# Performance work log

Hardware: AMD Instinct MI355X
Metric: run time of the kernel (lower is better)

## Reference

```python
import jax, jax.numpy as jnp
import numpy as np

E, T, H, I = 32, 512, 2048, 768


def setup_inputs() -> dict:
    key = jax.random.key(0)
    k1, k2, k3, k4 = jax.random.split(key, 4)
    scale = 1.0 / np.sqrt(H)
    return {
        "routed_input": jax.random.normal(k1, (E, T, H), dtype=jnp.float32),
        "gate_proj": jax.random.normal(k2, (E, I, H), dtype=jnp.float32) * scale,
        "up_proj": jax.random.normal(k3, (E, I, H), dtype=jnp.float32) * scale,
        "down_proj": jax.random.normal(k4, (E, H, I), dtype=jnp.float32) * scale,
    }


def reference(routed_input, gate_proj, up_proj, down_proj):
    # routed_input: [E, T, H]; per-expert SwiGLU MLP, concat over experts.
    gate = jnp.einsum("eth,eih->eti", routed_input, gate_proj)
    up = jnp.einsum("eth,eih->eti", routed_input, up_proj)
    hidden = jax.nn.silu(gate) * up  # [E, T, I]
    out = jnp.einsum("eti,ehi->eth", hidden, down_proj)  # [E, T, H]
    return out.reshape(E * T, H)
```

## Files before the change

kernel.cpp:

```cpp
#include <hip/hip_runtime.h>


#define NE 32
#define NT 512
#define NH 2048
#define NI 768

typedef short        short8  __attribute__((ext_vector_type(8)));
typedef float        floatx4 __attribute__((ext_vector_type(4)));
typedef __attribute__((address_space(1))) const unsigned int g_u32;
typedef __attribute__((address_space(3))) unsigned int l_u32;

__device__ __forceinline__ void gl_lds16(const void* g, void* l) {
    __builtin_amdgcn_global_load_lds((g_u32*)g, (l_u32*)l, 16, 0, 0);
}

__device__ __forceinline__ unsigned int cvt_pk_bf16(float lo, float hi) {
    unsigned int r;
    asm("v_cvt_pk_bf16_f32 %0, %1, %2" : "=v"(r) : "v"(lo), "v"(hi));
    return r;
}

__device__ __forceinline__ short8 frag8(floatx4 x0, floatx4 x1) {
    union { unsigned int u[4]; short8 s; } t;
    t.u[0] = cvt_pk_bf16(x0[0], x0[1]);
    t.u[1] = cvt_pk_bf16(x0[2], x0[3]);
    t.u[2] = cvt_pk_bf16(x1[0], x1[1]);
    t.u[3] = cvt_pk_bf16(x1[2], x1[3]);
    return t.s;
}

__device__ __forceinline__ ushort f2bf(float f) {
    union { float f; unsigned int u; } v; v.f = f;
    unsigned int r = v.u + 0x7fffu + ((v.u >> 16) & 1u);
    return (ushort)(r >> 16);
}

__global__ __launch_bounds__(512, 1) void moe_gateup(
    const float* __restrict__ rin, const float* __restrict__ gate,
    const float* __restrict__ up, ushort* __restrict__ hidden)
{
    __shared__ float S[3][3][128][32];

    const int bid = blockIdx.x;
    const int wg  = (bid & 7) * 96 + (bid >> 3);
    const int e   = wg / 24;
    const int rem = wg % 24;
    const int ti  = rem % 6;
    const int tm  = rem / 6;

    const int tid  = threadIdx.x;
    const int lane = tid & 63;
    const int wave = tid >> 6;
    const int wr = wave >> 1;
    const int wc = wave & 1;

    const float* Ab = rin  + (size_t)e * NT * NH + (size_t)(tm * 128) * NH;
    const float* Gb = gate + (size_t)e * NI * NH + (size_t)(ti * 128) * NH;
    const float* Ub = up   + (size_t)e * NI * NH + (size_t)(ti * 128) * NH;

    floatx4 accg[2][4], accu[2][4];
    #pragma unroll
    for (int m = 0; m < 2; ++m)
        #pragma unroll
        for (int n = 0; n < 4; ++n) {
            accg[m][n] = (floatx4)0.f;
            accu[m][n] = (floatx4)0.f;
        }

    const int frow = lane & 15;
    const int h    = lane >> 4;
    const int KT = NH / 32;

#define STAGE(kt, b) do {                                                    \
        const int k0_ = (kt) * 32;                                           \
        _Pragma("unroll")                                                    \
        for (int i = 0; i < 6; ++i) {                                        \
            const int idx = wave * 6 + i;                                    \
            const int t_  = idx >> 4;                                        \
            const int ri  = idx & 15;                                        \
            const int r_  = ri * 8 + (lane >> 3);                            \
            const int cs_ = (lane & 7) ^ (r_ & 7);                           \
            const float* src = (t_ == 0 ? Ab : (t_ == 1 ? Gb : Ub))          \
                               + (size_t)r_ * NH + k0_ + cs_ * 4;            \
            gl_lds16(src, &S[b][t_][ri * 8][0]);                             \
        }                                                                    \
    } while (0)

    STAGE(0, 0);
    STAGE(1, 1);

    for (int kt = 0; kt < KT; ++kt) {
        const int cur = kt % 3;
        __builtin_amdgcn_s_barrier();
        if (kt + 2 < KT) {
            STAGE(kt + 2, (kt + 2) % 3);
            asm volatile("s_waitcnt vmcnt(12)" ::: "memory");
        } else if (kt + 1 < KT) {
            asm volatile("s_waitcnt vmcnt(6)" ::: "memory");
        } else {
            asm volatile("s_waitcnt vmcnt(0)" ::: "memory");
        }
        __builtin_amdgcn_s_barrier();

        short8 af[2], gf[4], uf[4];
        #pragma unroll
        for (int m = 0; m < 2; ++m) {
            const int R = wr * 32 + m * 16 + frow;
            const int p0 = (2 * h)     ^ (R & 7);
            const int p1 = (2 * h + 1) ^ (R & 7);
            af[m] = frag8(*(const floatx4*)&S[cur][0][R][p0 * 4],
                          *(const floatx4*)&S[cur][0][R][p1 * 4]);
        }
        #pragma unroll
        for (int n = 0; n < 4; ++n) {
            const int R = wc * 64 + n * 16 + frow;
            const int p0 = (2 * h)     ^ (R & 7);
            const int p1 = (2 * h + 1) ^ (R & 7);
            gf[n] = frag8(*(const floatx4*)&S[cur][1][R][p0 * 4],
                          *(const floatx4*)&S[cur][1][R][p1 * 4]);
            uf[n] = frag8(*(const floatx4*)&S[cur][2][R][p0 * 4],
                          *(const floatx4*)&S[cur][2][R][p1 * 4]);
        }
        #pragma unroll
        for (int m = 0; m < 2; ++m)
            #pragma unroll
            for (int n = 0; n < 4; ++n) {
                accg[m][n] = __builtin_amdgcn_mfma_f32_16x16x32_bf16(
                    af[m], gf[n], accg[m][n], 0, 0, 0);
                accu[m][n] = __builtin_amdgcn_mfma_f32_16x16x32_bf16(
                    af[m], uf[n], accu[m][n], 0, 0, 0);
            }

        asm volatile("s_waitcnt lgkmcnt(0)" ::: "memory");
        __builtin_amdgcn_sched_barrier(0);
    }
#undef STAGE

    const int ccol  = lane & 15;
    const int crow0 = (lane >> 4) * 4;
    const size_t hbase = ((size_t)e * NT + (size_t)tm * 128) * NI + ti * 128;
    #pragma unroll
    for (int m = 0; m < 2; ++m)
        #pragma unroll
        for (int n = 0; n < 4; ++n)
            #pragma unroll
            for (int j = 0; j < 4; ++j) {
                const float g = accg[m][n][j];
                const float u = accu[m][n][j];
                const float hh = (g / (1.f + __expf(-g))) * u;
                const int row = wr * 32 + m * 16 + crow0 + j;
                const int col = wc * 64 + n * 16 + ccol;
                hidden[hbase + (size_t)row * NI + col] = f2bf(hh);
            }
}

__global__ __launch_bounds__(256, 2) void moe_down(
    const ushort* __restrict__ hidden, const float* __restrict__ down,
    float* __restrict__ out)
{
    __shared__ ushort As[2][128][32];
    __shared__ float  Bs[2][128][32];

    const int bid = blockIdx.x;
    const int wg  = (bid & 7) * (2048 / 8) + (bid >> 3);
    const int e   = wg >> 6;
    const int rem = wg & 63;
    const int tn  = rem & 15;
    const int tm  = rem >> 4;

    const int tid  = threadIdx.x;
    const int lane = tid & 63;
    const int wave = tid >> 6;
    const int wr = wave >> 1, wc = wave & 1;

    const ushort* Ab = hidden + ((size_t)e * NT + (size_t)tm * 128) * NI;
    const float*  Bb = down + (size_t)e * NH * NI + (size_t)(tn * 128) * NI;

    floatx4 acc[4][4];
    #pragma unroll
    for (int m = 0; m < 4; ++m)
        #pragma unroll
        for (int n = 0; n < 4; ++n) acc[m][n] = (floatx4)0.f;

    const int frow = lane & 15;
    const int h    = lane >> 4;
    const int ca   = h ^ (frow & 3);
    const int rb   = frow & 7;
    const int c0   = (2 * h) ^ rb;
    const int c1   = (2 * h + 1) ^ rb;
    const int KT = NI / 32;

#define STAGE_DN(kt, b) do {                                                 \
        const int k0_ = (kt) * 32;                                           \
        _Pragma("unroll")                                                    \
        for (int i = 0; i < 2; ++i) {                                        \
            const int g_ = wave * 2 + i;                                     \
            const int r_ = g_ * 16 + (lane >> 2);                            \
            const int cs_ = (lane & 3) ^ (r_ & 3);                           \
            gl_lds16(Ab + (size_t)r_ * NI + k0_ + cs_ * 8, &As[b][g_ * 16][0]); \
        }                                                                    \
        _Pragma("unroll")                                                    \
        for (int i = 0; i < 4; ++i) {                                        \
            const int g_ = wave * 4 + i;                                     \
            const int r_ = g_ * 8 + (lane >> 3);                             \
            const int cs_ = (lane & 7) ^ (r_ & 7);                           \
            gl_lds16(Bb + (size_t)r_ * NI + k0_ + cs_ * 4, &Bs[b][g_ * 8][0]); \
        }                                                                    \
    } while (0)

    STAGE_DN(0, 0);

    for (int kt = 0; kt < KT; ++kt) {
        const int cur = kt & 1;
        if (kt + 1 < KT) {
            STAGE_DN(kt + 1, cur ^ 1);
            asm volatile("s_waitcnt vmcnt(6)" ::: "memory");
        } else {
            asm volatile("s_waitcnt vmcnt(0)" ::: "memory");
        }
        __builtin_amdgcn_s_barrier();

        short8 af[4], bf[4];
        #pragma unroll
        for (int m = 0; m < 4; ++m) {
            const int R = wr * 64 + m * 16 + frow;
            af[m] = *(const short8*)&As[cur][R][ca * 8];
        }
        #pragma unroll
        for (int n = 0; n < 4; ++n) {
            const int R = wc * 64 + n * 16 + frow;
            bf[n] = frag8(*(const floatx4*)&Bs[cur][R][c0 * 4],
                          *(const floatx4*)&Bs[cur][R][c1 * 4]);
        }
        #pragma unroll
        for (int m = 0; m < 4; ++m)
            #pragma unroll
            for (int n = 0; n < 4; ++n)
                acc[m][n] = __builtin_amdgcn_mfma_f32_16x16x32_bf16(
                    af[m], bf[n], acc[m][n], 0, 0, 0);

        asm volatile("s_waitcnt lgkmcnt(0)" ::: "memory");
        __builtin_amdgcn_sched_barrier(0);
        __builtin_amdgcn_s_barrier();
    }
#undef STAGE_DN

    const int ccol  = lane & 15;
    const int crow0 = (lane >> 4) * 4;
    float* Ob = out + ((size_t)e * NT + (size_t)tm * 128) * NH + tn * 128;
    #pragma unroll
    for (int m = 0; m < 4; ++m)
        #pragma unroll
        for (int n = 0; n < 4; ++n)
            #pragma unroll
            for (int j = 0; j < 4; ++j) {
                const int row = wr * 64 + m * 16 + crow0 + j;
                const int col = wc * 64 + n * 16 + ccol;
                Ob[(size_t)row * NH + col] = acc[m][n][j];
            }
}

extern "C" void kernel_launch(void* const* d_in, const int* in_sizes, int n_in,
                              void* d_out, int out_size, void* d_ws, size_t ws_size,
                              hipStream_t stream) {
    const float* rin  = (const float*)d_in[0];
    const float* gate = (const float*)d_in[1];
    const float* up   = (const float*)d_in[2];
    const float* down = (const float*)d_in[3];
    float* out = (float*)d_out;
    ushort* hidden = (ushort*)d_ws;

    moe_gateup<<<dim3(768), dim3(512), 0, stream>>>(rin, gate, up, hidden);
    moe_down<<<dim3(2048), dim3(256), 0, stream>>>(hidden, down, out);
}
```

Before: 356.4 us.

## Stage gate/up GEMM operands through registers with bf16 LDS and double buffering

Replaces direct global-to-LDS fp32 async loads (triple-buffered) in the gate/up kernel with register prefetch of fp32 values, conversion to bf16 once before writing to a double-buffered LDS. This halves LDS footprint and removes the per-wave redundant fp32-to-bf16 conversions on fragment reads, allowing single short8 LDS reads per fragment. Wave tiling changes from 4x2 to 2x4 layout (64x32 per wave). Risks: register pressure from held prefetch data and reduced latency hiding versus async LDS loads.

```diff
diff --git a/kernel.cpp b/kernel.cpp
--- a/kernel.cpp
+++ b/kernel.cpp
@@ -8,6 +8,7 @@
 
 typedef short        short8  __attribute__((ext_vector_type(8)));
 typedef float        floatx4 __attribute__((ext_vector_type(4)));
+typedef unsigned int uintx4  __attribute__((ext_vector_type(4)));
 typedef __attribute__((address_space(1))) const unsigned int g_u32;
 typedef __attribute__((address_space(3))) unsigned int l_u32;
 
@@ -30,6 +31,15 @@
     return t.s;
 }
 
+__device__ __forceinline__ uintx4 pack8(floatx4 x0, floatx4 x1) {
+    uintx4 u;
+    u[0] = cvt_pk_bf16(x0[0], x0[1]);
+    u[1] = cvt_pk_bf16(x0[2], x0[3]);
+    u[2] = cvt_pk_bf16(x1[0], x1[1]);
+    u[3] = cvt_pk_bf16(x1[2], x1[3]);
+    return u;
+}
+
 __device__ __forceinline__ ushort f2bf(float f) {
     union { float f; unsigned int u; } v; v.f = f;
     unsigned int r = v.u + 0x7fffu + ((v.u >> 16) & 1u);
@@ -40,7 +50,7 @@
     const float* __restrict__ rin, const float* __restrict__ gate,
     const float* __restrict__ up, ushort* __restrict__ hidden)
 {
-    __shared__ float S[3][3][128][32];
+    __shared__ ushort S[2][3][128][32];
 
     const int bid = blockIdx.x;
     const int wg  = (bid & 7) * 96 + (bid >> 3);
@@ -52,18 +62,25 @@
     const int tid  = threadIdx.x;
     const int lane = tid & 63;
     const int wave = tid >> 6;
-    const int wr = wave >> 1;
-    const int wc = wave & 1;
+    const int wr = wave >> 2;
+    const int wc = wave & 3;
 
     const float* Ab = rin  + (size_t)e * NT * NH + (size_t)(tm * 128) * NH;
     const float* Gb = gate + (size_t)e * NI * NH + (size_t)(ti * 128) * NH;
     const float* Ub = up   + (size_t)e * NI * NH + (size_t)(ti * 128) * NH;
 
-    floatx4 accg[2][4], accu[2][4];
-    #pragma unroll
-    for (int m = 0; m < 2; ++m)
-        #pragma unroll
-        for (int n = 0; n < 4; ++n) {
+    const int s_row = wave * 16 + (lane >> 2);
+    const int s_cl  = lane & 3;
+    const int s_c   = s_cl ^ (s_row & 3);
+    const float* As_src = Ab + (size_t)s_row * NH + s_c * 8;
+    const float* Gs_src = Gb + (size_t)s_row * NH + s_c * 8;
+    const float* Us_src = Ub + (size_t)s_row * NH + s_c * 8;
+
+    floatx4 accg[4][2], accu[4][2];
+    #pragma unroll
+    for (int m = 0; m < 4; ++m)
+        #pragma unroll
+        for (int n = 0; n < 2; ++n) {
             accg[m][n] = (floatx4)0.f;
             accu[m][n] = (floatx4)0.f;
         }
@@ -72,85 +89,90 @@
     const int h    = lane >> 4;
     const int KT = NH / 32;
 
-#define STAGE(kt, b) do {                                                    \
-        const int k0_ = (kt) * 32;                                           \
-        _Pragma("unroll")                                                    \
-        for (int i = 0; i < 6; ++i) {                                        \
-            const int idx = wave * 6 + i;                                    \
-            const int t_  = idx >> 4;                                        \
-            const int ri  = idx & 15;                                        \
-            const int r_  = ri * 8 + (lane >> 3);                            \
-            const int cs_ = (lane & 7) ^ (r_ & 7);                           \
-            const float* src = (t_ == 0 ? Ab : (t_ == 1 ? Gb : Ub))          \
-                               + (size_t)r_ * NH + k0_ + cs_ * 4;            \
-            gl_lds16(src, &S[b][t_][ri * 8][0]);                             \
-        }                                                                    \
-    } while (0)
-
-    STAGE(0, 0);
-    STAGE(1, 1);
-
-    for (int kt = 0; kt < KT; ++kt) {
-        const int cur = kt % 3;
-        __builtin_amdgcn_s_barrier();
-        if (kt + 2 < KT) {
-            STAGE(kt + 2, (kt + 2) % 3);
-            asm volatile("s_waitcnt vmcnt(12)" ::: "memory");
-        } else if (kt + 1 < KT) {
-            asm volatile("s_waitcnt vmcnt(6)" ::: "memory");
-        } else {
-            asm volatile("s_waitcnt vmcnt(0)" ::: "memory");
-        }
-        __builtin_amdgcn_s_barrier();
-
-        short8 af[2], gf[4], uf[4];
-        #pragma unroll
-        for (int m = 0; m < 2; ++m) {
-            const int R = wr * 32 + m * 16 + frow;
-            const int p0 = (2 * h)     ^ (R & 7);
-            const int p1 = (2 * h + 1) ^ (R & 7);
-            af[m] = frag8(*(const floatx4*)&S[cur][0][R][p0 * 4],
-                          *(const floatx4*)&S[cur][0][R][p1 * 4]);
-        }
-        #pragma unroll
-        for (int n = 0; n < 4; ++n) {
-            const int R = wc * 64 + n * 16 + frow;
-            const int p0 = (2 * h)     ^ (R & 7);
-            const int p1 = (2 * h + 1) ^ (R & 7);
-            gf[n] = frag8(*(const floatx4*)&S[cur][1][R][p0 * 4],
-                          *(const floatx4*)&S[cur][1][R][p1 * 4]);
-            uf[n] = frag8(*(const floatx4*)&S[cur][2][R][p0 * 4],
-                          *(const floatx4*)&S[cur][2][R][p1 * 4]);
-        }
-        #pragma unroll
-        for (int m = 0; m < 2; ++m)
-            #pragma unroll
-            for (int n = 0; n < 4; ++n) {
-                accg[m][n] = __builtin_amdgcn_mfma_f32_16x16x32_bf16(
-                    af[m], gf[n], accg[m][n], 0, 0, 0);
-                accu[m][n] = __builtin_amdgcn_mfma_f32_16x16x32_bf16(
-                    af[m], uf[n], accu[m][n], 0, 0, 0);
-            }
-
-        asm volatile("s_waitcnt lgkmcnt(0)" ::: "memory");
-        __builtin_amdgcn_sched_barrier(0);
+    floatx4 pA0[3][2], pA1[3][2];
+
+#define ISSUE(kt, P) do {                                                    \
+        const int k_ = (kt) * 32;                                            \
+        P[0][0] = *(const floatx4*)(As_src + k_);                            \
+        P[0][1] = *(const floatx4*)(As_src + k_ + 4);                        \
+        P[1][0] = *(const floatx4*)(Gs_src + k_);                            \
+        P[1][1] = *(const floatx4*)(Gs_src + k_ + 4);                        \
+        P[2][0] = *(const floatx4*)(Us_src + k_);                            \
+        P[2][1] = *(const floatx4*)(Us_src + k_ + 4);                        \
+    } while (0)
+
+#define WRITE(b, P) do {                                                     \
+        *(uintx4*)&S[b][0][s_row][s_cl * 8] = pack8(P[0][0], P[0][1]);       \
+        *(uintx4*)&S[b][1][s_row][s_cl * 8] = pack8(P[1][0], P[1][1]);       \
+        *(uintx4*)&S[b][2][s_row][s_cl * 8] = pack8(P[2][0], P[2][1]);       \
+    } while (0)
+
+#define COMPUTE(b) do {                                                      \
+        short8 af[4], gf[2], uf[2];                                          \
+        _Pragma("unroll")                                                    \
+        for (int m = 0; m < 4; ++m) {                                        \
+            const int R = wr * 64 + m * 16 + frow;                           \
+            const int p = h ^ (R & 3);                                       \
+            af[m] = *(const short8*)&S[b][0][R][p * 8];                      \
+        }                                                                    \
+        _Pragma("unroll")                                                    \
+        for (int n = 0; n < 2; ++n) {                                        \
+            const int R = wc * 32 + n * 16 + frow;                           \
+            const int p = h ^ (R & 3);                                       \
+            gf[n] = *(const short8*)&S[b][1][R][p * 8];                      \
+            uf[n] = *(const short8*)&S[b][2][R][p * 8];                      \
+        }                                                                    \
+        _Pragma("unroll")                                                    \
+        for (int m = 0; m < 4; ++m)                                          \
+            _Pragma("unroll")                                                \
+            for (int n = 0; n < 2; ++n) {                                    \
+                accg[m][n] = __builtin_amdgcn_mfma_f32_16x16x32_bf16(        \
+                    af[m], gf[n], accg[m][n], 0, 0, 0);                      \
+                accu[m][n] = __builtin_amdgcn_mfma_f32_16x16x32_bf16(        \
+                    af[m], uf[n], accu[m][n], 0, 0, 0);                      \
+            }                                                                \
+    } while (0)
+
+#define ENDBAR() do {                                                        \
+        asm volatile("s_waitcnt lgkmcnt(0)" ::: "memory");                   \
+        __builtin_amdgcn_sched_barrier(0);                                   \
+        __builtin_amdgcn_s_barrier();                                        \
+    } while (0)
+
+    ISSUE(0, pA0);
+    ISSUE(1, pA1);
+    WRITE(0, pA0);
+    ENDBAR();
+
+    for (int kt = 0; kt < KT; kt += 2) {
+        if (kt + 2 < KT) ISSUE(kt + 2, pA0);
+        WRITE(1, pA1);
+        COMPUTE(0);
+        ENDBAR();
+        if (kt + 3 < KT) ISSUE(kt + 3, pA1);
+        if (kt + 2 < KT) WRITE(0, pA0);
+        COMPUTE(1);
+        ENDBAR();
     }
-#undef STAGE
+#undef ISSUE
+#undef WRITE
+#undef COMPUTE
+#undef ENDBAR
 
     const int ccol  = lane & 15;
     const int crow0 = (lane >> 4) * 4;
     const size_t hbase = ((size_t)e * NT + (size_t)tm * 128) * NI + ti * 128;
     #pragma unroll
-    for (int m = 0; m < 2; ++m)
-        #pragma unroll
-        for (int n = 0; n < 4; ++n)
+    for (int m = 0; m < 4; ++m)
+        #pragma unroll
+        for (int n = 0; n < 2; ++n)
             #pragma unroll
             for (int j = 0; j < 4; ++j) {
                 const float g = accg[m][n][j];
                 const float u = accu[m][n][j];
                 const float hh = (g / (1.f + __expf(-g))) * u;
-                const int row = wr * 32 + m * 16 + crow0 + j;
-                const int col = wc * 64 + n * 16 + ccol;
+                const int row = wr * 64 + m * 16 + crow0 + j;
+                const int col = wc * 32 + n * 16 + ccol;
                 hidden[hbase + (size_t)row * NI + col] = f2bf(hh);
             }
 }
```

Result: no change. 349.6 us (-1.9%).
